# Performance work log

Hardware: AMD Instinct MI355X
Metric: run time of the kernel (lower is better)

## Reference

```python
import jax, jax.numpy as jnp
import numpy as np

GAMMA = -0.1
ZETA = 1.1
L = 2  # args.L: number of hard-concrete samples averaged per layer


def setup_inputs() -> dict:
    key = jax.random.key(0)
    ks = jax.random.split(key, 11)
    N, E, D, H1, HID, OUT = 100000, 1600000, 128, 16, 128, 64
    x = jax.random.normal(ks[0], (N, D), jnp.float32)
    row = jax.random.randint(ks[1], (E,), 0, N, jnp.int32)
    col = jax.random.randint(ks[2], (E,), 0, N, jnp.int32)
    # attention MLP params, stacked over the 2 GCN layers (both take D=128 inputs)
    nb_w = jax.random.normal(ks[3], (2, D, H1), jnp.float32) * (1.0 / np.sqrt(D))
    nb_b = jnp.zeros((2, H1), jnp.float32)
    self_w = jax.random.normal(ks[4], (2, D, H1), jnp.float32) * (1.0 / np.sqrt(D))
    self_b = jnp.zeros((2, H1), jnp.float32)
    att_w = jax.random.normal(ks[5], (2, 2 * H1, 1), jnp.float32) * (1.0 / np.sqrt(2 * H1))
    att_b = jnp.zeros((2, 1), jnp.float32)
    # GCN weights (no bias, Kipf-style)
    w_gcn0 = jax.random.normal(ks[6], (D, HID), jnp.float32) * (1.0 / np.sqrt(D))
    w_gcn1 = jax.random.normal(ks[7], (HID, OUT), jnp.float32) * (1.0 / np.sqrt(HID))
    return {"x": x, "row": row, "col": col,
            "nb_w": nb_w, "nb_b": nb_b, "self_w": self_w, "self_b": self_b,
            "att_w": att_w, "att_b": att_b, "w_gcn0": w_gcn0, "w_gcn1": w_gcn1}


def reference(x, row, col, nb_w, nb_b, self_w, self_b, att_w, att_b, w_gcn0, w_gcn1):
    N = x.shape[0]
    diag = jnp.arange(N, dtype=row.dtype)
    # adjacency + identity (assumes no self-loops in the random edge list, as in tf.sparse.add)
    rows_all = jnp.concatenate([row, diag])
    cols_all = jnp.concatenate([col, diag])
    gcn_ws = [w_gcn0, w_gcn1]
    acts = [jax.nn.relu, lambda a: a]
    for i in range(2):
        xs = []
        for _ in range(L):
            # per-edge attention logit (eval path: no dropout, no concrete noise)
            h1 = jax.nn.relu(x[row] @ nb_w[i] + nb_b[i])       # [E, H1]
            h2 = jax.nn.relu(x[col] @ self_w[i] + self_b[i])   # [E, H1]
            logit = jnp.concatenate([h1, h2], axis=1) @ att_w[i] + att_b[i]  # [E, 1]
            gate = jax.nn.sigmoid(logit[:, 0])
            mask = jnp.clip(gate * (ZETA - GAMMA) + GAMMA, 0.0, 1.0)          # [E]
            vals = jnp.concatenate([mask, jnp.ones(N, x.dtype)])              # [E+N]
            rowsum = jax.ops.segment_sum(vals, rows_all, num_segments=N)
            d_inv_sqrt = jnp.clip(rowsum ** -0.5, 0.0, 10.0)
            vals_n = vals * d_inv_sqrt[rows_all] * d_inv_sqrt[cols_all]
            # GraphConvolution: support @ (x @ W)
            h = x @ gcn_ws[i]                                                 # [N, dout]
            agg = jax.ops.segment_sum(vals_n[:, None] * h[cols_all], rows_all, num_segments=N)
            xs.append(acts[i](agg))
        x = jnp.mean(jnp.stack(xs), axis=0)
    return x
```

## Files before the change

kernel.cpp:

```cpp
#include <hip/hip_runtime.h>


typedef __attribute__((ext_vector_type(8))) short bf16x8;
typedef __attribute__((ext_vector_type(4))) float f32x4;

__device__ inline float bf_lo(uint32_t u) { return __uint_as_float(u << 16); }
__device__ inline float bf_hi(uint32_t u) { return __uint_as_float(u & 0xffff0000u); }
__device__ inline ushort bf1(float x) {
  uint32_t b = __float_as_uint(x);
  return (ushort)((b + 0x7fffu + ((b >> 16) & 1u)) >> 16);
}
__device__ inline uint32_t pack_bf2(float x, float y) {
  return (uint32_t)bf1(x) | ((uint32_t)bf1(y) << 16);
}
__device__ inline float maskfn(float logit) {
  float g = 1.f / (1.f + __expf(-logit));
  return fminf(fmaxf(fmaf(g, 1.2f, -0.1f), 0.f), 1.f);
}

__global__ __launch_bounds__(256) void k_cvt(const float* __restrict__ X,
                                             ushort* __restrict__ Xb, int n8) {
  int i = blockIdx.x * 256 + threadIdx.x;
  if (i >= n8) return;
  const float4* s = (const float4*)(X + (size_t)i * 8);
  float4 v0 = s[0], v1 = s[1];
  uint4 o;
  o.x = pack_bf2(v0.x, v0.y); o.y = pack_bf2(v0.z, v0.w);
  o.z = pack_bf2(v1.x, v1.y); o.w = pack_bf2(v1.z, v1.w);
  *(uint4*)(Xb + (size_t)i * 8) = o;
}

__global__ __launch_bounds__(256) void k_wpack(const float* __restrict__ w0,
                                               const float* __restrict__ w1,
                                               const float* __restrict__ nbw,
                                               const float* __restrict__ sfw,
                                               ushort* __restrict__ w0b,
                                               ushort* __restrict__ w1b,
                                               ushort* __restrict__ aW0,
                                               ushort* __restrict__ aW1) {
  int t = blockIdx.x * 256 + threadIdx.x;
  if (t < 16384) {
    int j = t & 7, l = (t >> 3) & 63, g = (t >> 9) & 3, ct = t >> 11;
    int k = g * 32 + (l >> 4) * 8 + j;
    w0b[t] = bf1(w0[k * 128 + ct * 16 + (l & 15)]);
  } else if (t < 24576) {
    int rem = t - 16384;
    int j = rem & 7, l = (rem >> 3) & 63, g = (rem >> 9) & 3, ct = rem >> 11;
    int k = g * 32 + (l >> 4) * 8 + j;
    w1b[rem] = bf1(w1[k * 64 + ct * 16 + (l & 15)]);
  } else if (t < 32768) {
    int rem = t - 24576;
    int layer = rem >> 12;
    int full = rem & 4095;
    int j = full & 7, l = (full >> 3) & 63, g = (full >> 9) & 3, ct = full >> 11;
    int k = g * 32 + (l >> 4) * 8 + j;
    const float* src = (ct == 0 ? nbw : sfw) + layer * 2048;
    ushort* dst = (layer == 0 ? aW0 : aW1);
    dst[full] = bf1(src[k * 16 + (l & 15)]);
  }
}

__global__ __launch_bounds__(256) void k_matt(const ushort* __restrict__ Xb,
                                              const ushort* __restrict__ Wp,
                                              const float* __restrict__ b1,
                                              const float* __restrict__ b2,
                                              const float* __restrict__ aw,
                                              const float* __restrict__ attb,
                                              float* __restrict__ s1,
                                              float* __restrict__ s2, int N) {
  int tid = threadIdx.x, w = tid >> 6, l = tid & 63;
  int n0 = blockIdx.x * 64 + w * 16;
  int arow = n0 + (l & 15);
  if (arow >= N) arow = N - 1;
  const ushort* xr = Xb + (size_t)arow * 128 + (l >> 4) * 8;
  bf16x8 a[4];
#pragma unroll
  for (int g = 0; g < 4; ++g) a[g] = *(const bf16x8*)(xr + g * 32);
  f32x4 acc0 = {0.f, 0.f, 0.f, 0.f}, acc1 = acc0;
  const ushort* wp = Wp + l * 8;
#pragma unroll
  for (int g = 0; g < 4; ++g) {
    bf16x8 b0 = *(const bf16x8*)(wp + (size_t)g * 512);
    bf16x8 b1f = *(const bf16x8*)(wp + (size_t)(4 + g) * 512);
    acc0 = __builtin_amdgcn_mfma_f32_16x16x32_bf16(a[g], b0, acc0, 0, 0, 0);
    acc1 = __builtin_amdgcn_mfma_f32_16x16x32_bf16(a[g], b1f, acc1, 0, 0, 0);
  }
  int coln = l & 15;
  float awn = aw[coln], aws = aw[16 + coln];
  float bb1 = b1[coln], bb2 = b2[coln];
  float v1[4], v2[4];
#pragma unroll
  for (int r = 0; r < 4; ++r) {
    v1[r] = fmaxf(acc0[r] + bb1, 0.f) * awn;
    v2[r] = fmaxf(acc1[r] + bb2, 0.f) * aws;
  }
#pragma unroll
  for (int off = 1; off < 16; off <<= 1) {
#pragma unroll
    for (int r = 0; r < 4; ++r) {
      v1[r] += __shfl_xor(v1[r], off);
      v2[r] += __shfl_xor(v2[r], off);
    }
  }
  if (coln == 0) {
    int r0 = n0 + (l >> 4) * 4;
    float ab = attb[0];
#pragma unroll
    for (int r = 0; r < 4; ++r) {
      int row = r0 + r;
      if (row < N) { s1[row] = v1[r]; s2[row] = v2[r] + ab; }
    }
  }
}

template <int DOUT>
__global__ __launch_bounds__(256) void k_mgemm(const ushort* __restrict__ Xb,
                                               const ushort* __restrict__ Wp,
                                               const float* __restrict__ dis,
                                               ushort* __restrict__ H, int N) {
  constexpr int NCT = DOUT / 16;
  int tid = threadIdx.x, w = tid >> 6, l = tid & 63;
  int n0 = blockIdx.x * 64 + w * 16;
  int arow = n0 + (l & 15);
  if (arow >= N) arow = N - 1;
  const ushort* xr = Xb + (size_t)arow * 128 + (l >> 4) * 8;
  bf16x8 a[4];
#pragma unroll
  for (int g = 0; g < 4; ++g) a[g] = *(const bf16x8*)(xr + g * 32);
  f32x4 acc[NCT];
#pragma unroll
  for (int ct = 0; ct < NCT; ++ct) acc[ct] = (f32x4){0.f, 0.f, 0.f, 0.f};
  const ushort* wp = Wp + l * 8;
#pragma unroll
  for (int ct = 0; ct < NCT; ++ct) {
#pragma unroll
    for (int g = 0; g < 4; ++g) {
      bf16x8 b = *(const bf16x8*)(wp + (size_t)(ct * 4 + g) * 512);
      acc[ct] = __builtin_amdgcn_mfma_f32_16x16x32_bf16(a[g], b, acc[ct], 0, 0, 0);
    }
  }
  int r0 = n0 + (l >> 4) * 4;
  float scale[4];
#pragma unroll
  for (int r = 0; r < 4; ++r) scale[r] = (r0 + r < N) ? dis[r0 + r] : 0.f;
  int coln = l & 15;
#pragma unroll
  for (int ct = 0; ct < NCT; ++ct) {
    int col = ct * 16 + coln;
#pragma unroll
    for (int r = 0; r < 4; ++r) {
      int row = r0 + r;
      if (row < N) H[(size_t)row * DOUT + col] = bf1(acc[ct][r] * scale[r]);
    }
  }
}

__global__ __launch_bounds__(256) void k_hist8(const int* __restrict__ row,
                                               int* __restrict__ counts, int E, int N) {
  int g = blockIdx.x & 7;
  int bj = blockIdx.x >> 3, nbj = gridDim.x >> 3;
  int lo = (int)(((long long)N * g) >> 3);
  int hi = (int)(((long long)N * (g + 1)) >> 3);
  for (int e = bj * 256 + threadIdx.x; e < E; e += nbj * 256) {
    int r = row[e];
    if (r >= lo && r < hi) atomicAdd(&counts[r], 1);
  }
}

__global__ __launch_bounds__(256) void k_blocksum(const int* __restrict__ counts,
                                                  int* __restrict__ bsum, int N) {
  __shared__ int sdata[256];
  int base = blockIdx.x * 1024;
  int s = 0;
#pragma unroll
  for (int k = 0; k < 4; k++) {
    int i = base + k * 256 + threadIdx.x;
    if (i < N) s += counts[i];
  }
  sdata[threadIdx.x] = s;
  __syncthreads();
  for (int off = 128; off > 0; off >>= 1) {
    if (threadIdx.x < off) sdata[threadIdx.x] += sdata[threadIdx.x + off];
    __syncthreads();
  }
  if (threadIdx.x == 0) bsum[blockIdx.x] = sdata[0];
}

__global__ __launch_bounds__(128) void k_scanpart(const int* __restrict__ bsum,
                                                  int* __restrict__ boff, int NB,
                                                  int* __restrict__ row_start, int N) {
  __shared__ int s[129];
  int t = threadIdx.x;
  s[t] = (t < NB) ? bsum[t] : 0;
  __syncthreads();
  if (t == 0) {
    int r = 0;
    for (int b = 0; b < NB; b++) { int v = s[b]; s[b] = r; r += v; }
    row_start[N] = r;
  }
  __syncthreads();
  if (t < NB) boff[t] = s[t];
}

__global__ __launch_bounds__(256) void k_scanblk(const int* __restrict__ counts,
                                                 const int* __restrict__ boff,
                                                 int* __restrict__ row_start, int N) {
  __shared__ int warp_sums[4];
  int tid = threadIdx.x, lane = tid & 63, wid = tid >> 6;
  int base = blockIdx.x * 1024;
  int i0 = base + tid * 4;
  int c0, c1, c2, c3;
  if (i0 + 3 < N) {
    int4 v = *(const int4*)(counts + i0);
    c0 = v.x; c1 = v.y; c2 = v.z; c3 = v.w;
  } else {
    c0 = (i0 + 0 < N) ? counts[i0 + 0] : 0;
    c1 = (i0 + 1 < N) ? counts[i0 + 1] : 0;
    c2 = (i0 + 2 < N) ? counts[i0 + 2] : 0;
    c3 = (i0 + 3 < N) ? counts[i0 + 3] : 0;
  }
  int s = c0 + c1 + c2 + c3;
  int incl = s;
#pragma unroll
  for (int off = 1; off < 64; off <<= 1) {
    int v = __shfl_up(incl, off);
    if (lane >= off) incl += v;
  }
  if (lane == 63) warp_sums[wid] = incl;
  __syncthreads();
  int pre = 0;
  for (int w = 0; w < wid; w++) pre += warp_sums[w];
  int run = boff[blockIdx.x] + pre + incl - s;
  if (i0 + 0 < N) row_start[i0 + 0] = run; run += c0;
  if (i0 + 1 < N) row_start[i0 + 1] = run; run += c1;
  if (i0 + 2 < N) row_start[i0 + 2] = run; run += c2;
  if (i0 + 3 < N) row_start[i0 + 3] = run;
}

__global__ __launch_bounds__(256) void k_scatter8(const int* __restrict__ row,
                                                  const int* __restrict__ col,
                                                  const int* __restrict__ row_start,
                                                  int* __restrict__ counts,
                                                  int* __restrict__ csr_col, int E, int N) {
  int g = blockIdx.x & 7;
  int bj = blockIdx.x >> 3, nbj = gridDim.x >> 3;
  int lo = (int)(((long long)N * g) >> 3);
  int hi = (int)(((long long)N * (g + 1)) >> 3);
  for (int e = bj * 256 + threadIdx.x; e < E; e += nbj * 256) {
    int r = row[e];
    if (r >= lo && r < hi) {
      int c = col[e];
      int old = atomicSub(&counts[r], 1);
      csr_col[row_start[r] + old - 1] = c;
    }
  }
}

__global__ __launch_bounds__(256) void k_mask(const int* __restrict__ rs,
                                              const int* __restrict__ csr_col,
                                              const float* __restrict__ s1,
                                              const float* __restrict__ s2,
                                              float* __restrict__ mask,
                                              float* __restrict__ dis, int N) {
  int lane = threadIdx.x & 63, wid = threadIdx.x >> 6;
  int sub = lane >> 4, sl = lane & 15;
  int r = blockIdx.x * 16 + wid * 4 + sub;
  if (r >= N) return;
  int start = rs[r], end = rs[r + 1];
  float s1r = s1[r];
  float sum = 0.f;
  for (int p = start + sl; p < end; p += 16) {
    float m = maskfn(s1r + s2[csr_col[p]]);
    mask[p] = m;
    sum += m;
  }
#pragma unroll
  for (int off = 1; off < 16; off <<= 1) sum += __shfl_xor(sum, off);
  if (sl == 0) dis[r] = rsqrtf(sum + 1.0f);
}

template <int DOUT, bool RELU, bool OUT_BF16>
__global__ __launch_bounds__(256) void k_agg(const int* __restrict__ rs,
                                             const int* __restrict__ csr_col,
                                             const float* __restrict__ mask,
                                             const float* __restrict__ dis,
                                             const uint32_t* __restrict__ Hs,
                                             void* __restrict__ outv, int N) {
  constexpr int LPE = DOUT / 8;
  constexpr int EPI = 64 / LPE;
  constexpr int RW = DOUT / 2;
  int lane = threadIdx.x & 63, wid = threadIdx.x >> 6;
  int r = blockIdx.x * 4 + wid;
  if (r >= N) return;
  int start = rs[r], end = rs[r + 1];
  int sub = lane / LPE;
  int fl = lane & (LPE - 1);
  float a0 = 0.f, a1 = 0.f, a2 = 0.f, a3 = 0.f, a4 = 0.f, a5 = 0.f, a6 = 0.f, a7 = 0.f;
  if (sub == 0) {
    uint4 u = *(const uint4*)(Hs + (size_t)r * RW + fl * 4);
    a0 = bf_lo(u.x); a1 = bf_hi(u.x); a2 = bf_lo(u.y); a3 = bf_hi(u.y);
    a4 = bf_lo(u.z); a5 = bf_hi(u.z); a6 = bf_lo(u.w); a7 = bf_hi(u.w);
  }
  int p = start;
  for (; p + 2 * EPI <= end; p += 2 * EPI) {
    int eA = p + sub, eB = p + EPI + sub;
    int cA = csr_col[eA], cB = csr_col[eB];
    float mA = mask[eA], mB = mask[eB];
    uint4 uA = *(const uint4*)(Hs + (size_t)cA * RW + fl * 4);
    uint4 uB = *(const uint4*)(Hs + (size_t)cB * RW + fl * 4);
    a0 = fmaf(mA, bf_lo(uA.x), a0); a1 = fmaf(mA, bf_hi(uA.x), a1);
    a2 = fmaf(mA, bf_lo(uA.y), a2); a3 = fmaf(mA, bf_hi(uA.y), a3);
    a4 = fmaf(mA, bf_lo(uA.z), a4); a5 = fmaf(mA, bf_hi(uA.z), a5);
    a6 = fmaf(mA, bf_lo(uA.w), a6); a7 = fmaf(mA, bf_hi(uA.w), a7);
    a0 = fmaf(mB, bf_lo(uB.x), a0); a1 = fmaf(mB, bf_hi(uB.x), a1);
    a2 = fmaf(mB, bf_lo(uB.y), a2); a3 = fmaf(mB, bf_hi(uB.y), a3);
    a4 = fmaf(mB, bf_lo(uB.z), a4); a5 = fmaf(mB, bf_hi(uB.z), a5);
    a6 = fmaf(mB, bf_lo(uB.w), a6); a7 = fmaf(mB, bf_hi(uB.w), a7);
  }
  for (; p < end; p += EPI) {
    int e = p + sub;
    bool v = e < end;
    int c = v ? csr_col[e] : r;
    float m = v ? mask[e] : 0.f;
    uint4 u = *(const uint4*)(Hs + (size_t)c * RW + fl * 4);
    a0 = fmaf(m, bf_lo(u.x), a0); a1 = fmaf(m, bf_hi(u.x), a1);
    a2 = fmaf(m, bf_lo(u.y), a2); a3 = fmaf(m, bf_hi(u.y), a3);
    a4 = fmaf(m, bf_lo(u.z), a4); a5 = fmaf(m, bf_hi(u.z), a5);
    a6 = fmaf(m, bf_lo(u.w), a6); a7 = fmaf(m, bf_hi(u.w), a7);
  }
#pragma unroll
  for (int off = LPE; off < 64; off <<= 1) {
    a0 += __shfl_xor(a0, off); a1 += __shfl_xor(a1, off);
    a2 += __shfl_xor(a2, off); a3 += __shfl_xor(a3, off);
    a4 += __shfl_xor(a4, off); a5 += __shfl_xor(a5, off);
    a6 += __shfl_xor(a6, off); a7 += __shfl_xor(a7, off);
  }
  if (lane < LPE) {
    float dr = dis[r];
    float o[8] = {dr * a0, dr * a1, dr * a2, dr * a3, dr * a4, dr * a5, dr * a6, dr * a7};
    if (RELU) {
#pragma unroll
      for (int q = 0; q < 8; ++q) o[q] = fmaxf(o[q], 0.f);
    }
    if (OUT_BF16) {
      uint4 u;
      u.x = pack_bf2(o[0], o[1]); u.y = pack_bf2(o[2], o[3]);
      u.z = pack_bf2(o[4], o[5]); u.w = pack_bf2(o[6], o[7]);
      *(uint4*)((uint32_t*)outv + (size_t)r * RW + fl * 4) = u;
    } else {
      float* op = (float*)outv + (size_t)r * DOUT + fl * 8;
      *(float4*)op = make_float4(o[0], o[1], o[2], o[3]);
      *(float4*)(op + 4) = make_float4(o[4], o[5], o[6], o[7]);
    }
  }
}

extern "C" void kernel_launch(void* const* d_in, const int* in_sizes, int n_in,
                              void* d_out, int out_size, void* d_ws, size_t ws_size,
                              hipStream_t stream) {
  const float* x      = (const float*)d_in[0];
  const int*   row    = (const int*)d_in[1];
  const int*   col    = (const int*)d_in[2];
  const float* nb_w   = (const float*)d_in[3];
  const float* nb_b   = (const float*)d_in[4];
  const float* self_w = (const float*)d_in[5];
  const float* self_b = (const float*)d_in[6];
  const float* att_w  = (const float*)d_in[7];
  const float* att_b  = (const float*)d_in[8];
  const float* w0     = (const float*)d_in[9];
  const float* w1     = (const float*)d_in[10];
  float* out = (float*)d_out;

  const int N = in_sizes[0] / 128;
  const int E = in_sizes[1];

  char* wp = (char*)d_ws;
  auto alloc = [&](size_t bytes) -> void* {
    void* q = (void*)wp;
    wp += (bytes + 255) & ~(size_t)255;
    return q;
  };
  int*      counts    = (int*)alloc((size_t)N * 4);
  int*      row_start = (int*)alloc((size_t)(N + 1) * 4);
  int*      bsum      = (int*)alloc(512);
  int*      boff      = (int*)alloc(512);
  int*      csr_col   = (int*)alloc((size_t)E * 4);
  float*    mask      = (float*)alloc((size_t)E * 4);
  float*    s1        = (float*)alloc((size_t)N * 4);
  float*    s2        = (float*)alloc((size_t)N * 4);
  float*    dis       = (float*)alloc((size_t)N * 4);
  ushort*   xb        = (ushort*)alloc((size_t)N * 128 * 2);
  ushort*   Hs        = (ushort*)alloc((size_t)N * 128 * 2);
  ushort*   w0b       = (ushort*)alloc(16384 * 2);
  ushort*   w1b       = (ushort*)alloc(8192 * 2);
  ushort*   aW0       = (ushort*)alloc(4096 * 2);
  ushort*   aW1       = (ushort*)alloc(4096 * 2);

  const int NB = (N + 1023) / 1024;
  const int gw = (N + 3) / 4;
  const int gk = (N + 15) / 16;
  const int gm = (N + 63) / 64;
  const int gc = (N * 16 + 255) / 256;

  hipMemsetAsync(counts, 0, (size_t)N * 4, stream);
  k_hist8<<<2048, 256, 0, stream>>>(row, counts, E, N);
  k_blocksum<<<NB, 256, 0, stream>>>(counts, bsum, N);
  k_scanpart<<<1, 128, 0, stream>>>(bsum, boff, NB, row_start, N);
  k_scanblk<<<NB, 256, 0, stream>>>(counts, boff, row_start, N);
  k_scatter8<<<2048, 256, 0, stream>>>(row, col, row_start, counts, csr_col, E, N);
  k_cvt<<<gc, 256, 0, stream>>>(x, xb, N * 16);
  k_wpack<<<128, 256, 0, stream>>>(w0, w1, nb_w, self_w, w0b, w1b, aW0, aW1);

  k_matt<<<gm, 256, 0, stream>>>(xb, aW0, nb_b, self_b, att_w, att_b, s1, s2, N);
  k_mask<<<gk, 256, 0, stream>>>(row_start, csr_col, s1, s2, mask, dis, N);
  k_mgemm<128><<<gm, 256, 0, stream>>>(xb, w0b, dis, Hs, N);
  k_agg<128, true, true><<<gw, 256, 0, stream>>>(row_start, csr_col, mask, dis,
                                                 (const uint32_t*)Hs, xb, N);

  k_matt<<<gm, 256, 0, stream>>>(xb, aW1, nb_b + 16, self_b + 16, att_w + 32, att_b + 1,
                                 s1, s2, N);
  k_mask<<<gk, 256, 0, stream>>>(row_start, csr_col, s1, s2, mask, dis, N);
  k_mgemm<64><<<gm, 256, 0, stream>>>(xb, w1b, dis, Hs, N);
  k_agg<64, false, false><<<gw, 256, 0, stream>>>(row_start, csr_col, mask, dis,
                                                  (const uint32_t*)Hs, out, N);
}
```

Measured before the change: 445.9 us.

## Build CSR via two-pass bucket partition with shared-memory histograms and scatter

```diff
diff --git a/kernel.cpp b/kernel.cpp
--- a/kernel.cpp
+++ b/kernel.cpp
@@ -1,5 +1,7 @@
 #include <hip/hip_runtime.h>
 
+
+#define NBKT 64
 
 typedef __attribute__((ext_vector_type(8))) short bf16x8;
 typedef __attribute__((ext_vector_type(4))) float f32x4;
@@ -16,6 +18,158 @@
 __device__ inline float maskfn(float logit) {
   float g = 1.f / (1.f + __expf(-logit));
   return fminf(fmaxf(fmaf(g, 1.2f, -0.1f), 0.f), 1.f);
+}
+
+__global__ __launch_bounds__(256) void k_binA(const int* __restrict__ row,
+                                              const int* __restrict__ col,
+                                              int rpp, int E, int PCAP,
+                                              uint32_t* __restrict__ part,
+                                              int* __restrict__ gcur) {
+  __shared__ int cnt[NBKT];
+  __shared__ int base[NBKT];
+  int tid = threadIdx.x;
+  if (tid < NBKT) cnt[tid] = 0;
+  __syncthreads();
+  int e0 = blockIdx.x * 1024;
+  int r[4], c[4], b[4];
+  bool v[4];
+#pragma unroll
+  for (int q = 0; q < 4; ++q) {
+    int e = e0 + q * 256 + tid;
+    v[q] = e < E;
+    if (v[q]) {
+      r[q] = __builtin_nontemporal_load(row + e);
+      c[q] = __builtin_nontemporal_load(col + e);
+      b[q] = r[q] / rpp;
+      atomicAdd(&cnt[b[q]], 1);
+    }
+  }
+  __syncthreads();
+  if (tid < NBKT) {
+    int n = cnt[tid];
+    base[tid] = n ? atomicAdd(&gcur[tid], n) : 0;
+    cnt[tid] = 0;
+  }
+  __syncthreads();
+#pragma unroll
+  for (int q = 0; q < 4; ++q) {
+    if (v[q]) {
+      int rank = atomicAdd(&cnt[b[q]], 1);
+      part[(size_t)b[q] * PCAP + base[b[q]] + rank] =
+          ((uint32_t)(r[q] - b[q] * rpp) << 17) | (uint32_t)c[q];
+    }
+  }
+}
+
+__global__ __launch_bounds__(1024) void k_bhist(const uint32_t* __restrict__ part,
+                                                const int* __restrict__ gcur,
+                                                int rpp, int N, int PCAP,
+                                                int* __restrict__ counts) {
+  __shared__ int h[2048];
+  int tid = threadIdx.x, b = blockIdx.x;
+  for (int i = tid; i < rpp; i += 1024) h[i] = 0;
+  __syncthreads();
+  int n = gcur[b];
+  const uint32_t* my = part + (size_t)b * PCAP;
+  for (int i = tid; i < n; i += 1024) atomicAdd(&h[my[i] >> 17], 1);
+  __syncthreads();
+  int r0 = b * rpp;
+  for (int i = tid; i < rpp; i += 1024)
+    if (r0 + i < N) counts[r0 + i] = h[i];
+}
+
+__global__ __launch_bounds__(1024) void k_bscat(const uint32_t* __restrict__ part,
+                                                const int* __restrict__ gcur,
+                                                const int* __restrict__ row_start,
+                                                int rpp, int N, int PCAP,
+                                                int* __restrict__ csr_col) {
+  __shared__ int cur[2048];
+  __shared__ int rs[2048];
+  int tid = threadIdx.x, b = blockIdx.x;
+  int r0 = b * rpp;
+  for (int i = tid; i < rpp; i += 1024) {
+    cur[i] = 0;
+    rs[i] = (r0 + i < N) ? row_start[r0 + i] : 0;
+  }
+  __syncthreads();
+  int n = gcur[b];
+  const uint32_t* my = part + (size_t)b * PCAP;
+  for (int i = tid; i < n; i += 1024) {
+    uint32_t u = my[i];
+    int rl = u >> 17;
+    int pos = rs[rl] + atomicAdd(&cur[rl], 1);
+    csr_col[pos] = (int)(u & 0x1FFFFu);
+  }
+}
+
+__global__ __launch_bounds__(256) void k_blocksum(const int* __restrict__ counts,
+                                                  int* __restrict__ bsum, int N) {
+  __shared__ int sdata[256];
+  int base = blockIdx.x * 1024;
+  int s = 0;
+#pragma unroll
+  for (int k = 0; k < 4; k++) {
+    int i = base + k * 256 + threadIdx.x;
+    if (i < N) s += counts[i];
+  }
+  sdata[threadIdx.x] = s;
+  __syncthreads();
+  for (int off = 128; off > 0; off >>= 1) {
+    if (threadIdx.x < off) sdata[threadIdx.x] += sdata[threadIdx.x + off];
+    __syncthreads();
+  }
+  if (threadIdx.x == 0) bsum[blockIdx.x] = sdata[0];
+}
+
+__global__ __launch_bounds__(128) void k_scanpart(const int* __restrict__ bsum,
+                                                  int* __restrict__ boff, int NB,
+                                                  int* __restrict__ row_start, int N) {
+  __shared__ int s[129];
+  int t = threadIdx.x;
+  s[t] = (t < NB) ? bsum[t] : 0;
+  __syncthreads();
+  if (t == 0) {
+    int r = 0;
+    for (int b = 0; b < NB; b++) { int v = s[b]; s[b] = r; r += v; }
+    row_start[N] = r;
+  }
+  __syncthreads();
+  if (t < NB) boff[t] = s[t];
+}
+
+__global__ __launch_bounds__(256) void k_scanblk(const int* __restrict__ counts,
+                                                 const int* __restrict__ boff,
+                                                 int* __restrict__ row_start, int N) {
+  __shared__ int warp_sums[4];
+  int tid = threadIdx.x, lane = tid & 63, wid = tid >> 6;
+  int base = blockIdx.x * 1024;
+  int i0 = base + tid * 4;
+  int c0, c1, c2, c3;
+  if (i0 + 3 < N) {
+    int4 v = *(const int4*)(counts + i0);
+    c0 = v.x; c1 = v.y; c2 = v.z; c3 = v.w;
+  } else {
+    c0 = (i0 + 0 < N) ? counts[i0 + 0] : 0;
+    c1 = (i0 + 1 < N) ? counts[i0 + 1] : 0;
+    c2 = (i0 + 2 < N) ? counts[i0 + 2] : 0;
+    c3 = (i0 + 3 < N) ? counts[i0 + 3] : 0;
+  }
+  int s = c0 + c1 + c2 + c3;
+  int incl = s;
+#pragma unroll
+  for (int off = 1; off < 64; off <<= 1) {
+    int v = __shfl_up(incl, off);
+    if (lane >= off) incl += v;
+  }
+  if (lane == 63) warp_sums[wid] = incl;
+  __syncthreads();
+  int pre = 0;
+  for (int w = 0; w < wid; w++) pre += warp_sums[w];
+  int run = boff[blockIdx.x] + pre + incl - s;
+  if (i0 + 0 < N) row_start[i0 + 0] = run; run += c0;
+  if (i0 + 1 < N) row_start[i0 + 1] = run; run += c1;
+  if (i0 + 2 < N) row_start[i0 + 2] = run; run += c2;
+  if (i0 + 3 < N) row_start[i0 + 3] = run;
 }
 
 __global__ __launch_bounds__(256) void k_cvt(const float* __restrict__ X,
@@ -155,107 +309,6 @@
   }
 }
 
-__global__ __launch_bounds__(256) void k_hist8(const int* __restrict__ row,
-                                               int* __restrict__ counts, int E, int N) {
-  int g = blockIdx.x & 7;
-  int bj = blockIdx.x >> 3, nbj = gridDim.x >> 3;
-  int lo = (int)(((long long)N * g) >> 3);
-  int hi = (int)(((long long)N * (g + 1)) >> 3);
-  for (int e = bj * 256 + threadIdx.x; e < E; e += nbj * 256) {
-    int r = row[e];
-    if (r >= lo && r < hi) atomicAdd(&counts[r], 1);
-  }
-}
-
-__global__ __launch_bounds__(256) void k_blocksum(const int* __restrict__ counts,
-                                                  int* __restrict__ bsum, int N) {
-  __shared__ int sdata[256];
-  int base = blockIdx.x * 1024;
-  int s = 0;
-#pragma unroll
-  for (int k = 0; k < 4; k++) {
-    int i = base + k * 256 + threadIdx.x;
-    if (i < N) s += counts[i];
-  }
-  sdata[threadIdx.x] = s;
-  __syncthreads();
-  for (int off = 128; off > 0; off >>= 1) {
-    if (threadIdx.x < off) sdata[threadIdx.x] += sdata[threadIdx.x + off];
-    __syncthreads();
-  }
-  if (threadIdx.x == 0) bsum[blockIdx.x] = sdata[0];
-}
-
-__global__ __launch_bounds__(128) void k_scanpart(const int* __restrict__ bsum,
-                                                  int* __restrict__ boff, int NB,
-                                                  int* __restrict__ row_start, int N) {
-  __shared__ int s[129];
-  int t = threadIdx.x;
-  s[t] = (t < NB) ? bsum[t] : 0;
-  __syncthreads();
-  if (t == 0) {
-    int r = 0;
-    for (int b = 0; b < NB; b++) { int v = s[b]; s[b] = r; r += v; }
-    row_start[N] = r;
-  }
-  __syncthreads();
-  if (t < NB) boff[t] = s[t];
-}
-
-__global__ __launch_bounds__(256) void k_scanblk(const int* __restrict__ counts,
-                                                 const int* __restrict__ boff,
-                                                 int* __restrict__ row_start, int N) {
-  __shared__ int warp_sums[4];
-  int tid = threadIdx.x, lane = tid & 63, wid = tid >> 6;
-  int base = blockIdx.x * 1024;
-  int i0 = base + tid * 4;
-  int c0, c1, c2, c3;
-  if (i0 + 3 < N) {
-    int4 v = *(const int4*)(counts + i0);
-    c0 = v.x; c1 = v.y; c2 = v.z; c3 = v.w;
-  } else {
-    c0 = (i0 + 0 < N) ? counts[i0 + 0] : 0;
-    c1 = (i0 + 1 < N) ? counts[i0 + 1] : 0;
-    c2 = (i0 + 2 < N) ? counts[i0 + 2] : 0;
-    c3 = (i0 + 3 < N) ? counts[i0 + 3] : 0;
-  }
-  int s = c0 + c1 + c2 + c3;
-  int incl = s;
-#pragma unroll
-  for (int off = 1; off < 64; off <<= 1) {
-    int v = __shfl_up(incl, off);
-    if (lane >= off) incl += v;
-  }
-  if (lane == 63) warp_sums[wid] = incl;
-  __syncthreads();
-  int pre = 0;
-  for (int w = 0; w < wid; w++) pre += warp_sums[w];
-  int run = boff[blockIdx.x] + pre + incl - s;
-  if (i0 + 0 < N) row_start[i0 + 0] = run; run += c0;
-  if (i0 + 1 < N) row_start[i0 + 1] = run; run += c1;
-  if (i0 + 2 < N) row_start[i0 + 2] = run; run += c2;
-  if (i0 + 3 < N) row_start[i0 + 3] = run;
-}
-
-__global__ __launch_bounds__(256) void k_scatter8(const int* __restrict__ row,
-                                                  const int* __restrict__ col,
-                                                  const int* __restrict__ row_start,
-                                                  int* __restrict__ counts,
-                                                  int* __restrict__ csr_col, int E, int N) {
-  int g = blockIdx.x & 7;
-  int bj = blockIdx.x >> 3, nbj = gridDim.x >> 3;
-  int lo = (int)(((long long)N * g) >> 3);
-  int hi = (int)(((long long)N * (g + 1)) >> 3);
-  for (int e = bj * 256 + threadIdx.x; e < E; e += nbj * 256) {
-    int r = row[e];
-    if (r >= lo && r < hi) {
-      int c = col[e];
-      int old = atomicSub(&counts[r], 1);
-      csr_col[row_start[r] + old - 1] = c;
-    }
-  }
-}
-
 __global__ __launch_bounds__(256) void k_mask(const int* __restrict__ rs,
                                               const int* __restrict__ csr_col,
                                               const float* __restrict__ s1,
@@ -373,6 +426,8 @@
 
   const int N = in_sizes[0] / 128;
   const int E = in_sizes[1];
+  const int rpp = (N + NBKT - 1) / NBKT;
+  const int PCAP = (((E / NBKT) + 4096 + 255) / 256) * 256;
 
   char* wp = (char*)d_ws;
   auto alloc = [&](size_t bytes) -> void* {
@@ -384,6 +439,7 @@
   int*      row_start = (int*)alloc((size_t)(N + 1) * 4);
   int*      bsum      = (int*)alloc(512);
   int*      boff      = (int*)alloc(512);
+  int*      gcur      = (int*)alloc(NBKT * 4);
   int*      csr_col   = (int*)alloc((size_t)E * 4);
   float*    mask      = (float*)alloc((size_t)E * 4);
   float*    s1        = (float*)alloc((size_t)N * 4);
@@ -395,19 +451,22 @@
   ushort*   w1b       = (ushort*)alloc(8192 * 2);
   ushort*   aW0       = (ushort*)alloc(4096 * 2);
   ushort*   aW1       = (ushort*)alloc(4096 * 2);
+  uint32_t* part      = (uint32_t*)Hs;
 
   const int NB = (N + 1023) / 1024;
   const int gw = (N + 3) / 4;
   const int gk = (N + 15) / 16;
   const int gm = (N + 63) / 64;
   const int gc = (N * 16 + 255) / 256;
-
-  hipMemsetAsync(counts, 0, (size_t)N * 4, stream);
-  k_hist8<<<2048, 256, 0, stream>>>(row, counts, E, N);
+  const int gA = (E + 1023) / 1024;
+
+  hipMemsetAsync(gcur, 0, NBKT * 4, stream);
+  k_binA<<<gA, 256, 0, stream>>>(row, col, rpp, E, PCAP, part, gcur);
+  k_bhist<<<NBKT, 1024, 0, stream>>>(part, gcur, rpp, N, PCAP, counts);
   k_blocksum<<<NB, 256, 0, stream>>>(counts, bsum, N);
   k_scanpart<<<1, 128, 0, stream>>>(bsum, boff, NB, row_start, N);
   k_scanblk<<<NB, 256, 0, stream>>>(counts, boff, row_start, N);
-  k_scatter8<<<2048, 256, 0, stream>>>(row, col, row_start, counts, csr_col, E, N);
+  k_bscat<<<NBKT, 1024, 0, stream>>>(part, gcur, row_start, rpp, N, PCAP, csr_col);
   k_cvt<<<gc, 256, 0, stream>>>(x, xb, N * 16);
   k_wpack<<<128, 256, 0, stream>>>(w0, w1, nb_w, self_w, w0b, w1b, aW0, aW1);
 
```

After: 372.8 us. 1.2x faster.
